# Optimization experiments

Hardware: AMD Instinct MI355X
Metric: run time of the kernel (lower is better)

Reference implementation:

```python
import jax, jax.numpy as jnp
import numpy as np

N = 32768          # total nodes
B = 64             # graphs
NPG = N // B       # nodes per graph (equal-sized graphs)
E = 524288         # edges (before self-loops)
D_IN, HID, HEADS, D_OUT = 128, 64, 4, 128
DH = HID * HEADS   # 256
NEG_SLOPE = 0.2
EPS = 1e-5

def _leaky(x):
    return jnp.where(x >= 0, x, NEG_SLOPE * x)

def gat_conv(x, src, dst, W, a_src, a_dst, b, concat):
    """PyG-style GATConv (self-loops already included in src/dst)."""
    H, C = a_src.shape
    h = (x @ W).reshape(N, H, C)                       # [N,H,C]
    es = jnp.einsum('nhc,hc->nh', h, a_src)            # score from source feats
    ed = jnp.einsum('nhc,hc->nh', h, a_dst)            # score from target feats
    e = _leaky(es[src] + ed[dst])                      # [E',H]
    m = jax.ops.segment_max(e, dst, num_segments=N)    # stable softmax per dst
    p = jnp.exp(e - m[dst])
    s = jax.ops.segment_sum(p, dst, num_segments=N)
    alpha = p / s[dst]                                 # [E',H]
    out = jax.ops.segment_sum(h[src] * alpha[..., None], dst, num_segments=N)
    out = out.reshape(N, H * C) if concat else out.mean(axis=1)
    return out + b

def mha(x, Wi, bi, Wo, bo, heads):
    """torch.nn.MultiheadAttention (batch_first, no mask, eval)."""
    Bb, T, D = x.shape
    qkv = x @ Wi.T + bi                                # [B,T,3D]
    q, k, v = jnp.split(qkv, 3, axis=-1)
    hd = D // heads
    def sp(t):
        return t.reshape(Bb, T, heads, hd).transpose(0, 2, 1, 3)  # [B,h,T,hd]
    q, k, v = sp(q), sp(k), sp(v)
    scores = jnp.einsum('bhqd,bhkd->bhqk', q, k) / jnp.sqrt(jnp.float32(hd))
    attn = jax.nn.softmax(scores, axis=-1)
    o = jnp.einsum('bhqk,bhkd->bhqd', attn, v)
    o = o.transpose(0, 2, 1, 3).reshape(Bb, T, D)
    return o @ Wo.T + bo

def layer_norm(x, g, b):
    mu = x.mean(-1, keepdims=True)
    var = x.var(-1, keepdims=True)
    return (x - mu) / jnp.sqrt(var + EPS) * g + b

def setup_inputs() -> dict:
    key = jax.random.key(0)
    ks = jax.random.split(key, 20)
    s = 0.1
    inp = {
        'x': jax.random.normal(ks[0], (N, D_IN), jnp.float32),
        'edge_index': jax.random.randint(ks[1], (2, E), 0, N, jnp.int64),
        'batch': (jnp.arange(N, dtype=jnp.int64) // NPG),
        # gat1: D_IN -> HEADS*HID (concat)
        'W1': jax.random.normal(ks[2], (D_IN, HEADS * HID), jnp.float32) * s,
        'aS1': jax.random.normal(ks[3], (HEADS, HID), jnp.float32) * s,
        'aD1': jax.random.normal(ks[4], (HEADS, HID), jnp.float32) * s,
        'b1': jnp.zeros((HEADS * HID,), jnp.float32),
        # gat2: DH -> HEADS*HID (concat)
        'W2': jax.random.normal(ks[5], (DH, HEADS * HID), jnp.float32) * s,
        'aS2': jax.random.normal(ks[6], (HEADS, HID), jnp.float32) * s,
        'aD2': jax.random.normal(ks[7], (HEADS, HID), jnp.float32) * s,
        'b2': jnp.zeros((HEADS * HID,), jnp.float32),
        # gat3: DH -> D_OUT, heads=1, concat=False (mean)
        'W3': jax.random.normal(ks[8], (DH, D_OUT), jnp.float32) * s,
        'aS3': jax.random.normal(ks[9], (1, D_OUT), jnp.float32) * s,
        'aD3': jax.random.normal(ks[10], (1, D_OUT), jnp.float32) * s,
        'b3': jnp.zeros((D_OUT,), jnp.float32),
        # MultiheadAttention
        'Wi': jax.random.normal(ks[11], (3 * DH, DH), jnp.float32) * s,
        'bi': jnp.zeros((3 * DH,), jnp.float32),
        'Wo': jax.random.normal(ks[12], (DH, DH), jnp.float32) * s,
        'bo': jnp.zeros((DH,), jnp.float32),
        # LayerNorm
        'gamma': jnp.ones((DH,), jnp.float32),
        'beta': jnp.zeros((DH,), jnp.float32),
    }
    return inp

def reference(x, edge_index, batch, W1, aS1, aD1, b1, W2, aS2, aD2, b2,
              W3, aS3, aD3, b3, Wi, bi, Wo, bo, gamma, beta):
    # add self-loops (PyG GATConv default)
    loops = jnp.arange(N, dtype=edge_index.dtype)
    src = jnp.concatenate([edge_index[0], loops])
    dst = jnp.concatenate([edge_index[1], loops])

    x1 = jax.nn.elu(gat_conv(x, src, dst, W1, aS1, aD1, b1, concat=True))
    x2 = jax.nn.elu(gat_conv(x1, src, dst, W2, aS2, aD2, b2, concat=True))

    # ragged-to-dense batching: batch = arange(N)//NPG (equal-sized, sorted),
    # so the torch python loop reduces to a reshape with no padding.
    x2b = x2.reshape(B, NPG, DH)
    attended = mha(x2b, Wi, bi, Wo, bo, HEADS).reshape(N, DH)

    x2a = layer_norm(attended + x2, gamma, beta)
    x3 = gat_conv(x2a, src, dst, W3, aS3, aD3, b3, concat=False)
    return x3
```

## Files before the change

### kernel.cpp

```cpp
#include <hip/hip_runtime.h>

typedef _Float16 half_t;
typedef _Float16 half8  __attribute__((ext_vector_type(8)));
typedef _Float16 half4v __attribute__((ext_vector_type(4)));
typedef float    f32x4  __attribute__((ext_vector_type(4)));

constexpr int N_NODES = 32768;
constexpr int NPG_    = 512;

#define MFMA16(a, b, c) __builtin_amdgcn_mfma_f32_16x16x32_f16((a), (b), (c), 0, 0, 0)

__device__ __forceinline__ void gload_lds16(const half_t* g, half_t* l) {
  __builtin_amdgcn_global_load_lds(
      (const __attribute__((address_space(1))) void*)g,
      (__attribute__((address_space(3))) void*)l, 16, 0, 0);
}

__global__ void k_hist(const int* __restrict__ dst, int* __restrict__ deg, int E) {
  int i = blockIdx.x * 256 + threadIdx.x;
  if (i < E) atomicAdd(&deg[dst[i]], 1);
}

__global__ __launch_bounds__(1024) void k_scan(const int* __restrict__ deg,
                                               int* __restrict__ rowptr) {
  __shared__ int part[1024];
  int t = threadIdx.x;
  int base = t * 32;
  int s = 0;
  #pragma unroll
  for (int i = 0; i < 32; i++) s += deg[base + i];
  part[t] = s;
  __syncthreads();
  for (int off = 1; off < 1024; off <<= 1) {
    int add = (t >= off) ? part[t - off] : 0;
    __syncthreads();
    part[t] += add;
    __syncthreads();
  }
  int run = (t == 0) ? 0 : part[t - 1];
  for (int i = 0; i < 32; i++) { rowptr[base + i] = run; run += deg[base + i]; }
  if (t == 1023) rowptr[N_NODES] = run;
}

__global__ void k_selfloop(const int* __restrict__ rowptr, int* __restrict__ fill,
                           int* __restrict__ col) {
  int i = blockIdx.x * 256 + threadIdx.x;
  fill[i] = 1;
  col[rowptr[i]] = i;
}

__global__ void k_scatter(const int* __restrict__ src, const int* __restrict__ dst,
                          const int* __restrict__ rowptr, int* __restrict__ fill,
                          int* __restrict__ col, int E) {
  int i = blockIdx.x * 256 + threadIdx.x;
  if (i < E) {
    int d = dst[i];
    int pos = rowptr[d] + atomicAdd(&fill[d], 1);
    col[pos] = src[i];
  }
}

__global__ void k_convert(
    const float* __restrict__ x,  half_t* __restrict__ x_h,
    const float* __restrict__ W1, half_t* __restrict__ W1t,
    const float* __restrict__ W2, half_t* __restrict__ W2t,
    const float* __restrict__ W3, half_t* __restrict__ W3t,
    const float* __restrict__ Wi, half_t* __restrict__ Wi_h,
    const float* __restrict__ Wo, half_t* __restrict__ Wo_h,
    int* __restrict__ deg)
{
  int bid = blockIdx.x, t = threadIdx.x;
  if (bid < 16384) {
    int i = bid * 256 + t;
    x_h[i] = (half_t)x[i];
  } else if (bid < 16512) {
    int i = (bid - 16384) * 256 + t;
    int o = i >> 7, k = i & 127;
    W1t[i] = (half_t)W1[k * 256 + o];
  } else if (bid < 16768) {
    int i = (bid - 16512) * 256 + t;
    int o = i >> 8, k = i & 255;
    W2t[i] = (half_t)W2[k * 256 + o];
  } else if (bid < 16896) {
    int i = (bid - 16768) * 256 + t;
    int o = i >> 8, k = i & 255;
    W3t[i] = (half_t)W3[k * 128 + o];
  } else if (bid < 17664) {
    int i = (bid - 16896) * 256 + t;
    Wi_h[i] = (half_t)Wi[i];
  } else if (bid < 17920) {
    int i = (bid - 17664) * 256 + t;
    Wo_h[i] = (half_t)Wo[i];
  } else {
    deg[(bid - 17920) * 256 + t] = 1;
  }
}

__global__ __launch_bounds__(256) void k_gemm(
    const half_t* __restrict__ A, const half_t* __restrict__ Bt,
    const float* __restrict__ bias, int bias_per_row,
    half_t* __restrict__ outh, float* __restrict__ outf,
    int M, int Nc, int K,
    const float* __restrict__ aS, const float* __restrict__ aD,
    float* __restrict__ es, float* __restrict__ ed, int H)
{
  __shared__ __align__(16) half_t As[128 * 64];
  __shared__ __align__(16) half_t Bs[128 * 64];
  __shared__ float sRed[2][4][64];
  int w = threadIdx.x >> 6, lane = threadIdx.x & 63;
  int r = lane & 15, q = lane >> 4;
  int m0 = blockIdx.y * 128, n0 = blockIdx.x * 128;
  int mh = (w & 1) * 64, nh = (w >> 1) * 64;
  f32x4 acc[4][4];
  #pragma unroll
  for (int i = 0; i < 4; i++)
    #pragma unroll
    for (int j = 0; j < 4; j++) acc[i][j] = f32x4{0.f, 0.f, 0.f, 0.f};

  int srow = lane >> 3;
  int sc   = lane & 7;

  for (int k0 = 0; k0 < K; k0 += 64) {
    __syncthreads();
    #pragma unroll
    for (int i = 0; i < 4; i++) {
      int R0 = w * 32 + i * 8;
      int row = R0 + srow;
      int cg = sc ^ (row & 7);
      gload_lds16(A  + (size_t)(m0 + row) * K + k0 + cg * 8, &As[R0 * 64]);
      gload_lds16(Bt + (size_t)(n0 + row) * K + k0 + cg * 8, &Bs[R0 * 64]);
    }
    __syncthreads();
    #pragma unroll
    for (int kk = 0; kk < 2; kk++) {
      half8 af[4], bf[4];
      #pragma unroll
      for (int t = 0; t < 4; t++) {
        int rr = mh + t * 16 + r;
        af[t] = *(const half8*)&As[rr * 64 + (((kk * 4 + q) ^ (rr & 7)) << 3)];
      }
      #pragma unroll
      for (int t = 0; t < 4; t++) {
        int rr = nh + t * 16 + r;
        bf[t] = *(const half8*)&Bs[rr * 64 + (((kk * 4 + q) ^ (rr & 7)) << 3)];
      }
      #pragma unroll
      for (int ti = 0; ti < 4; ti++)
        #pragma unroll
        for (int tj = 0; tj < 4; tj++)
          acc[ti][tj] = MFMA16(af[ti], bf[tj], acc[ti][tj]);
    }
  }

  #pragma unroll
  for (int tj = 0; tj < 4; tj++) {
    int colc = n0 + nh + tj * 16 + r;
    #pragma unroll
    for (int ti = 0; ti < 4; ti++) {
      #pragma unroll
      for (int i = 0; i < 4; i++) {
        int row = m0 + mh + ti * 16 + q * 4 + i;
        float bv = bias ? (bias_per_row ? bias[row] : bias[colc]) : 0.f;
        float v = acc[ti][tj][i] + bv;
        size_t idx = (size_t)row * Nc + colc;
        if (outf) outf[idx] = v;
        if (outh) outh[idx] = (half_t)v;
      }
    }
  }

  if (es) {
    if (H == 4) {
      int head = (n0 >> 6) + (nh >> 6);
      float aSv[4], aDv[4];
      #pragma unroll
      for (int tj = 0; tj < 4; tj++) {
        int cl = tj * 16 + r;
        aSv[tj] = aS[head * 64 + cl];
        aDv[tj] = aD[head * 64 + cl];
      }
      #pragma unroll
      for (int ti = 0; ti < 4; ti++) {
        #pragma unroll
        for (int i = 0; i < 4; i++) {
          float ps = 0.f, pd = 0.f;
          #pragma unroll
          for (int tj = 0; tj < 4; tj++) {
            float av = acc[ti][tj][i];
            ps += av * aSv[tj];
            pd += av * aDv[tj];
          }
          #pragma unroll
          for (int off = 1; off < 16; off <<= 1) {
            ps += __shfl_xor(ps, off);
            pd += __shfl_xor(pd, off);
          }
          if (r == 0) {
            int row = m0 + mh + ti * 16 + q * 4 + i;
            es[(size_t)row * 4 + head] = ps;
            ed[(size_t)row * 4 + head] = pd;
          }
        }
      }
    } else {
      float aSv[4], aDv[4];
      #pragma unroll
      for (int tj = 0; tj < 4; tj++) {
        int c = nh + tj * 16 + r;
        aSv[tj] = aS[c];
        aDv[tj] = aD[c];
      }
      #pragma unroll
      for (int ti = 0; ti < 4; ti++) {
        #pragma unroll
        for (int i = 0; i < 4; i++) {
          float ps = 0.f, pd = 0.f;
          #pragma unroll
          for (int tj = 0; tj < 4; tj++) {
            float av = acc[ti][tj][i];
            ps += av * aSv[tj];
            pd += av * aDv[tj];
          }
          #pragma unroll
          for (int off = 1; off < 16; off <<= 1) {
            ps += __shfl_xor(ps, off);
            pd += __shfl_xor(pd, off);
          }
          if (r == 0) {
            int ri = ti * 16 + q * 4 + i;
            sRed[0][w][ri] = ps;
            sRed[1][w][ri] = pd;
          }
        }
      }
      __syncthreads();
      if (threadIdx.x < 128) {
        int row = threadIdx.x;
        int wlo = row >> 6, ri = row & 63;
        es[m0 + row] = sRed[0][wlo][ri] + sRed[0][wlo + 2][ri];
        ed[m0 + row] = sRed[1][wlo][ri] + sRed[1][wlo + 2][ri];
      }
    }
  }
}

template<int HC, int H, bool FP16ACC>
__global__ __launch_bounds__(256) void k_agg(
    const half_t* __restrict__ h, const float* __restrict__ es,
    const float* __restrict__ ed, const float* __restrict__ bias,
    const int* __restrict__ rowptr, const int* __restrict__ col, int elu,
    float* __restrict__ outf, half_t* __restrict__ outh)
{
  constexpr int VPT = HC / 16;
  constexpr int NV8 = VPT / 8;
  constexpr int C = HC / H;
  int lane = threadIdx.x & 63;
  int g = lane >> 4, li = lane & 15;
  int n = blockIdx.x * 4 + (threadIdx.x >> 6);
  int cbase = li * VPT;
  int hl = cbase / C;
  float edn = ed[(size_t)n * H + hl];
  int j0 = rowptr[n], j1 = rowptr[n + 1];
  const half_t* hb = h + cbase;

  float sum0 = 0.f, sum1 = 0.f;

  if constexpr (FP16ACC) {
    half8 acc0[NV8], acc1[NV8];
    #pragma unroll
    for (int i = 0; i < NV8; i++) {
      acc0[i] = half8{0, 0, 0, 0, 0, 0, 0, 0};
      acc1[i] = half8{0, 0, 0, 0, 0, 0, 0, 0};
    }
    for (int j = j0 + g; j < j1; j += 8) {
      int jb = j + 4;
      int s0 = col[j];
      int s1 = col[(jb < j1) ? jb : j];
      float e0 = es[(size_t)s0 * H + hl] + edn;
      e0 = fmaxf(e0, 0.2f * e0);
      float e1 = es[(size_t)s1 * H + hl] + edn;
      e1 = fmaxf(e1, 0.2f * e1);
      e1 = (jb < j1) ? e1 : -1e30f;
      const half_t* hp0 = hb + (size_t)s0 * HC;
      const half_t* hp1 = hb + (size_t)s1 * HC;
      float p0 = __expf(e0 - 6.f), p1 = __expf(e1 - 6.f);
      sum0 += p0; sum1 += p1;
      half_t q0 = (half_t)p0, q1 = (half_t)p1;
      half8 pv0 = {q0, q0, q0, q0, q0, q0, q0, q0};
      half8 pv1 = {q1, q1, q1, q1, q1, q1, q1, q1};
      #pragma unroll
      for (int i = 0; i < NV8; i++) {
        half8 v0 = *(const half8*)(hp0 + i * 8);
        half8 v1 = *(const half8*)(hp1 + i * 8);
        acc0[i] += pv0 * v0;
        acc1[i] += pv1 * v1;
      }
    }
    float sum = sum0 + sum1;
    sum += __shfl_xor(sum, 16);
    sum += __shfl_xor(sum, 32);
    float av[VPT];
    #pragma unroll
    for (int i = 0; i < VPT; i++) {
      av[i] = (float)acc0[i >> 3][i & 7] + (float)acc1[i >> 3][i & 7];
      av[i] += __shfl_xor(av[i], 16);
      av[i] += __shfl_xor(av[i], 32);
    }
    float inv = 1.f / sum;
    float v[VPT];
    #pragma unroll
    for (int i = 0; i < VPT; i++) {
      float t = av[i] * inv + bias[cbase + i];
      if (elu) t = (t > 0.f) ? t : __expf(t) - 1.f;
      v[i] = t;
    }
    if (g == 0) {
      size_t obase = (size_t)n * HC + cbase;
      if (outh) {
        #pragma unroll
        for (int p8 = 0; p8 < NV8; p8++) {
          half8 hv;
          #pragma unroll
          for (int i = 0; i < 8; i++) hv[i] = (half_t)v[p8 * 8 + i];
          *(half8*)(outh + obase + p8 * 8) = hv;
        }
      }
      if (outf) {
        #pragma unroll
        for (int p4 = 0; p4 < VPT / 4; p4++) {
          float4 fv = {v[p4 * 4], v[p4 * 4 + 1], v[p4 * 4 + 2], v[p4 * 4 + 3]};
          *(float4*)(outf + obase + p4 * 4) = fv;
        }
      }
    }
  } else {
    float acc0[VPT], acc1[VPT];
    #pragma unroll
    for (int i = 0; i < VPT; i++) { acc0[i] = 0.f; acc1[i] = 0.f; }
    for (int j = j0 + g; j < j1; j += 8) {
      int jb = j + 4;
      int s0 = col[j];
      int s1 = col[(jb < j1) ? jb : j];
      float e0 = es[(size_t)s0 * H + hl] + edn;
      e0 = fmaxf(e0, 0.2f * e0);
      float e1 = es[(size_t)s1 * H + hl] + edn;
      e1 = fmaxf(e1, 0.2f * e1);
      e1 = (jb < j1) ? e1 : -1e30f;
      const half_t* hp0 = hb + (size_t)s0 * HC;
      const half_t* hp1 = hb + (size_t)s1 * HC;
      float p0 = __expf(e0), p1 = __expf(e1);
      sum0 += p0; sum1 += p1;
      #pragma unroll
      for (int c8 = 0; c8 < NV8; c8++) {
        half8 a0 = *(const half8*)(hp0 + c8 * 8);
        half8 a1 = *(const half8*)(hp1 + c8 * 8);
        #pragma unroll
        for (int i = 0; i < 8; i++) {
          acc0[c8 * 8 + i] += p0 * (float)a0[i];
          acc1[c8 * 8 + i] += p1 * (float)a1[i];
        }
      }
    }
    float sum = sum0 + sum1;
    sum += __shfl_xor(sum, 16);
    sum += __shfl_xor(sum, 32);
    float av[VPT];
    #pragma unroll
    for (int i = 0; i < VPT; i++) {
      av[i] = acc0[i] + acc1[i];
      av[i] += __shfl_xor(av[i], 16);
      av[i] += __shfl_xor(av[i], 32);
    }
    float inv = 1.f / sum;
    float v[VPT];
    #pragma unroll
    for (int i = 0; i < VPT; i++) {
      float t = av[i] * inv + bias[cbase + i];
      if (elu) t = (t > 0.f) ? t : __expf(t) - 1.f;
      v[i] = t;
    }
    if (g == 0) {
      size_t obase = (size_t)n * HC + cbase;
      if (outh) {
        #pragma unroll
        for (int p8 = 0; p8 < NV8; p8++) {
          half8 hv;
          #pragma unroll
          for (int i = 0; i < 8; i++) hv[i] = (half_t)v[p8 * 8 + i];
          *(half8*)(outh + obase + p8 * 8) = hv;
        }
      }
      if (outf) {
        #pragma unroll
        for (int p4 = 0; p4 < VPT / 4; p4++) {
          float4 fv = {v[p4 * 4], v[p4 * 4 + 1], v[p4 * 4 + 2], v[p4 * 4 + 3]};
          *(float4*)(outf + obase + p4 * 4) = fv;
        }
      }
    }
  }
}

__global__ __launch_bounds__(256) void k_attn(
    const half_t* __restrict__ qk, const half_t* __restrict__ vt,
    half_t* __restrict__ o)
{
  __shared__ __align__(16) half_t Kt[128 * 64];
  __shared__ __align__(16) half_t Vt[64 * 128];
  __shared__ __align__(16) half_t Pb[4][16][136];

  int pair = blockIdx.x;
  int b = pair >> 2, hh = pair & 3;
  int q0 = blockIdx.y * 64;
  int w = threadIdx.x >> 6, lane = threadIdx.x & 63;
  int cc = lane & 15, qq = lane >> 4;

  const half_t* Qp = qk + ((size_t)(b * NPG_ + q0 + w * 16 + cc) * 512 + hh * 64);
  half8 qa0 = *(const half8*)(Qp + qq * 8);
  half8 qa1 = *(const half8*)(Qp + 32 + qq * 8);

  f32x4 oacc[4];
  #pragma unroll
  for (int t = 0; t < 4; t++) oacc[t] = f32x4{0.f, 0.f, 0.f, 0.f};
  float rs = 0.f;

  const half_t* kb = qk + ((size_t)(b * NPG_) * 512 + 256 + hh * 64);
  const half_t* vb = vt + ((size_t)(hh * 64) * 32768 + b * NPG_);

  int krow_l = lane >> 3, ks_l = lane & 7;
  int vrow_l = lane >> 4, vs_l = lane & 15;

  for (int kt = 0; kt < 4; kt++) {
    __syncthreads();
    #pragma unroll
    for (int i = 0; i < 4; i++) {
      int R = (i * 4 + w) * 8;
      int kr = R + krow_l;
      gload_lds16(kb + (size_t)(kt * 128 + kr) * 512 + ((ks_l ^ (kr & 7)) * 8),
                  &Kt[R * 64]);
    }
    #pragma unroll
    for (int i = 0; i < 4; i++) {
      int D0 = (i * 4 + w) * 4;
      int d = D0 + vrow_l;
      gload_lds16(vb + (size_t)d * 32768 + kt * 128 + ((vs_l ^ (d & 15)) * 8),
                  &Vt[D0 * 128]);
    }
    __syncthreads();

    #pragma unroll
    for (int mt = 0; mt < 8; mt++) {
      int key = mt * 16 + cc;
      half8 k0 = *(const half8*)&Kt[key * 64 + ((qq ^ (key & 7)) << 3)];
      half8 k1 = *(const half8*)&Kt[key * 64 + (((qq + 4) ^ (key & 7)) << 3)];
      f32x4 s = f32x4{0.f, 0.f, 0.f, 0.f};
      s = MFMA16(k0, qa0, s);
      s = MFMA16(k1, qa1, s);
      half4v ph;
      #pragma unroll
      for (int i = 0; i < 4; i++) {
        float p = __expf(s[i] * 0.125f - 8.0f);
        rs += p;
        ph[i] = (half_t)p;
      }
      *(half4v*)&Pb[w][cc][mt * 16 + qq * 4] = ph;
    }

    #pragma unroll
    for (int kc = 0; kc < 4; kc++) {
      half8 a = *(const half8*)&Pb[w][cc][kc * 32 + qq * 8];
      #pragma unroll
      for (int nt = 0; nt < 4; nt++) {
        int d = nt * 16 + cc;
        half8 bb = *(const half8*)&Vt[d * 128 + (((kc * 4 + qq) ^ (d & 15)) << 3)];
        oacc[nt] = MFMA16(a, bb, oacc[nt]);
      }
    }
  }

  rs += __shfl_xor(rs, 16);
  rs += __shfl_xor(rs, 32);
  #pragma unroll
  for (int i = 0; i < 4; i++) {
    float rsv = __shfl(rs, qq * 4 + i);
    float inv = 1.f / rsv;
    int node = b * NPG_ + q0 + w * 16 + qq * 4 + i;
    #pragma unroll
    for (int nt = 0; nt < 4; nt++)
      o[(size_t)node * 256 + hh * 64 + nt * 16 + cc] = (half_t)(oacc[nt][i] * inv);
  }
}

__global__ __launch_bounds__(256) void k_ln(
    const half_t* __restrict__ att, const half_t* __restrict__ x2,
    const float* __restrict__ gamma, const float* __restrict__ beta,
    half_t* __restrict__ outh)
{
  int lane = threadIdx.x & 63;
  int n = blockIdx.x * 4 + (threadIdx.x >> 6);
  size_t base = (size_t)n * 256 + lane * 4;
  half4v a  = *(const half4v*)(att + base);
  half4v xx = *(const half4v*)(x2 + base);
  float v[4];
  #pragma unroll
  for (int i = 0; i < 4; i++) v[i] = (float)a[i] + (float)xx[i];
  float s  = v[0] + v[1] + v[2] + v[3];
  float ss = v[0]*v[0] + v[1]*v[1] + v[2]*v[2] + v[3]*v[3];
  #pragma unroll
  for (int off = 1; off < 64; off <<= 1) {
    s  += __shfl_xor(s, off);
    ss += __shfl_xor(ss, off);
  }
  float mean = s * (1.f / 256.f);
  float var  = ss * (1.f / 256.f) - mean * mean;
  float rstd = rsqrtf(var + 1e-5f);
  #pragma unroll
  for (int i = 0; i < 4; i++) {
    int c = lane * 4 + i;
    outh[(size_t)n * 256 + c] = (half_t)((v[i] - mean) * rstd * gamma[c] + beta[c]);
  }
}

extern "C" void kernel_launch(void* const* d_in, const int* in_sizes, int n_in,
                              void* d_out, int out_size, void* d_ws, size_t ws_size,
                              hipStream_t stream)
{
  const float* x    = (const float*)d_in[0];
  const int*   ei   = (const int*)d_in[1];
  const float* W1   = (const float*)d_in[3];
  const float* aS1  = (const float*)d_in[4];
  const float* aD1  = (const float*)d_in[5];
  const float* b1   = (const float*)d_in[6];
  const float* W2   = (const float*)d_in[7];
  const float* aS2  = (const float*)d_in[8];
  const float* aD2  = (const float*)d_in[9];
  const float* b2   = (const float*)d_in[10];
  const float* W3   = (const float*)d_in[11];
  const float* aS3  = (const float*)d_in[12];
  const float* aD3  = (const float*)d_in[13];
  const float* b3   = (const float*)d_in[14];
  const float* Wi   = (const float*)d_in[15];
  const float* bi   = (const float*)d_in[16];
  const float* Wo   = (const float*)d_in[17];
  const float* bo   = (const float*)d_in[18];
  const float* gam  = (const float*)d_in[19];
  const float* bet  = (const float*)d_in[20];
  float* out = (float*)d_out;
  const int N = N_NODES;
  int E = in_sizes[1] / 2;

  char* ws = (char*)d_ws;
  size_t off = 0;
  auto alloc = [&](size_t bytes) -> void* {
    void* p = ws + off;
    off = (off + bytes + 255) & ~(size_t)255;
    return p;
  };
  half_t* x_h    = (half_t*)alloc((size_t)N * 128 * 2);
  half_t* h_h    = (half_t*)alloc((size_t)N * 256 * 2);
  half_t* x1_h   = (half_t*)alloc((size_t)N * 256 * 2);
  half_t* x2_h   = (half_t*)alloc((size_t)N * 256 * 2);
  half_t* qk_h   = (half_t*)alloc((size_t)N * 512 * 2);
  half_t* vt_h   = (half_t*)alloc((size_t)256 * N * 2);
  half_t* o_h    = (half_t*)alloc((size_t)N * 256 * 2);
  half_t* att_h  = (half_t*)alloc((size_t)N * 256 * 2);
  half_t* x2a_h  = (half_t*)alloc((size_t)N * 256 * 2);
  half_t* W1t    = (half_t*)alloc(256 * 128 * 2);
  half_t* W2t    = (half_t*)alloc(256 * 256 * 2);
  half_t* W3t    = (half_t*)alloc(128 * 256 * 2);
  half_t* Wi_h   = (half_t*)alloc(768 * 256 * 2);
  half_t* Wo_h   = (half_t*)alloc(256 * 256 * 2);
  float*  es     = (float*) alloc((size_t)N * 4 * 4);
  float*  ed     = (float*) alloc((size_t)N * 4 * 4);
  int*    deg    = (int*)   alloc((size_t)N * 4);
  int*    fill   = (int*)   alloc((size_t)N * 4);
  int*    rowptr = (int*)   alloc(((size_t)N + 1) * 4);
  int*    col    = (int*)   alloc((size_t)(N + E) * 4);

  const int* srcE = ei;
  const int* dstE = ei + E;

  k_convert<<<18048, 256, 0, stream>>>(x, x_h, W1, W1t, W2, W2t, W3, W3t,
                                       Wi, Wi_h, Wo, Wo_h, deg);
  k_hist<<<(E + 255) / 256, 256, 0, stream>>>(dstE, deg, E);
  k_scan<<<1, 1024, 0, stream>>>(deg, rowptr);
  k_selfloop<<<N / 256, 256, 0, stream>>>(rowptr, fill, col);
  k_scatter<<<(E + 255) / 256, 256, 0, stream>>>(srcE, dstE, rowptr, fill, col, E);

  k_gemm<<<dim3(2, N / 128), 256, 0, stream>>>(x_h, W1t, nullptr, 0, h_h, nullptr,
                                               N, 256, 128, aS1, aD1, es, ed, 4);
  k_agg<256, 4, true><<<N / 4, 256, 0, stream>>>(h_h, es, ed, b1, rowptr, col, 1, nullptr, x1_h);

  k_gemm<<<dim3(2, N / 128), 256, 0, stream>>>(x1_h, W2t, nullptr, 0, h_h, nullptr,
                                               N, 256, 256, aS2, aD2, es, ed, 4);
  k_agg<256, 4, true><<<N / 4, 256, 0, stream>>>(h_h, es, ed, b2, rowptr, col, 1, nullptr, x2_h);

  k_gemm<<<dim3(4, N / 128), 256, 0, stream>>>(x2_h, Wi_h, bi, 0, qk_h, nullptr,
                                               N, 512, 256, nullptr, nullptr, nullptr, nullptr, 0);
  k_gemm<<<dim3(N / 128, 2), 256, 0, stream>>>(Wi_h + 512 * 256, x2_h, bi + 512, 1,
                                               vt_h, nullptr, 256, N, 256,
                                               nullptr, nullptr, nullptr, nullptr, 0);
  k_attn<<<dim3(256, 8), 256, 0, stream>>>(qk_h, vt_h, o_h);
  k_gemm<<<dim3(2, N / 128), 256, 0, stream>>>(o_h, Wo_h, bo, 0, att_h, nullptr,
                                               N, 256, 256, nullptr, nullptr, nullptr, nullptr, 0);

  k_ln<<<N / 4, 256, 0, stream>>>(att_h, x2_h, gam, bet, x2a_h);

  k_gemm<<<dim3(1, N / 128), 256, 0, stream>>>(x2a_h, W3t, nullptr, 0, h_h, nullptr,
                                               N, 128, 256, aS3, aD3, es, ed, 1);
  k_agg<128, 1, false><<<N / 4, 256, 0, stream>>>(h_h, es, ed, b3, rowptr, col, 0, out, nullptr);
}
```

Measured before the change: 460.0 us.

## Fuse output projection with residual LayerNorm and widen attention query tiles

Adds a k_gemm_ln kernel that runs the Wo projection, adds bias and the residual, and applies LayerNorm in the epilogue with a cross-wave reduction in shared memory. This removes the separate LN kernel and the att_h round trip. The attention kernel now gives each wave four 16-query subtiles, so each K/V tile loaded into LDS is reused across 256 queries per block instead of 64, at the cost of more accumulator registers and fewer blocks. The exponentials are rewritten as exp2f with pre-scaled constants in both attention and aggregation.

```diff
diff --git a/kernel.cpp b/kernel.cpp
--- a/kernel.cpp
+++ b/kernel.cpp
@@ -244,6 +244,123 @@
   }
 }
 
+__global__ __launch_bounds__(256) void k_gemm_ln(
+    const half_t* __restrict__ A, const half_t* __restrict__ Bt,
+    const float* __restrict__ bias, const half_t* __restrict__ res,
+    const float* __restrict__ gamma, const float* __restrict__ beta,
+    half_t* __restrict__ outh)
+{
+  __shared__ __align__(16) half_t As[64 * 64];
+  __shared__ __align__(16) half_t Bs[256 * 64];
+  __shared__ float sSum[4][64], sSq[4][64];
+  __shared__ float sMR[64][2];
+  int w = threadIdx.x >> 6, lane = threadIdx.x & 63;
+  int r = lane & 15, q = lane >> 4;
+  int m0 = blockIdx.x * 64;
+  int nh = w * 64;
+  f32x4 acc[4][4];
+  #pragma unroll
+  for (int i = 0; i < 4; i++)
+    #pragma unroll
+    for (int j = 0; j < 4; j++) acc[i][j] = f32x4{0.f, 0.f, 0.f, 0.f};
+
+  int srow = lane >> 3, sc = lane & 7;
+
+  for (int k0 = 0; k0 < 256; k0 += 64) {
+    __syncthreads();
+    #pragma unroll
+    for (int i = 0; i < 2; i++) {
+      int R0 = w * 16 + i * 8;
+      int row = R0 + srow;
+      int cg = sc ^ (row & 7);
+      gload_lds16(A + (size_t)(m0 + row) * 256 + k0 + cg * 8, &As[R0 * 64]);
+    }
+    #pragma unroll
+    for (int i = 0; i < 8; i++) {
+      int R0 = w * 64 + i * 8;
+      int row = R0 + srow;
+      int cg = sc ^ (row & 7);
+      gload_lds16(Bt + (size_t)row * 256 + k0 + cg * 8, &Bs[R0 * 64]);
+    }
+    __syncthreads();
+    #pragma unroll
+    for (int kk = 0; kk < 2; kk++) {
+      half8 af[4], bf[4];
+      #pragma unroll
+      for (int t = 0; t < 4; t++) {
+        int rr = t * 16 + r;
+        af[t] = *(const half8*)&As[rr * 64 + (((kk * 4 + q) ^ (rr & 7)) << 3)];
+      }
+      #pragma unroll
+      for (int t = 0; t < 4; t++) {
+        int rr = nh + t * 16 + r;
+        bf[t] = *(const half8*)&Bs[rr * 64 + (((kk * 4 + q) ^ (rr & 7)) << 3)];
+      }
+      #pragma unroll
+      for (int ti = 0; ti < 4; ti++)
+        #pragma unroll
+        for (int tj = 0; tj < 4; tj++)
+          acc[ti][tj] = MFMA16(af[ti], bf[tj], acc[ti][tj]);
+    }
+  }
+
+  float gv[4], bv[4];
+  #pragma unroll
+  for (int tj = 0; tj < 4; tj++) {
+    int col = nh + tj * 16 + r;
+    gv[tj] = gamma[col];
+    bv[tj] = beta[col];
+  }
+  #pragma unroll
+  for (int ti = 0; ti < 4; ti++) {
+    #pragma unroll
+    for (int i = 0; i < 4; i++) {
+      int row = ti * 16 + q * 4 + i;
+      float s = 0.f, ss = 0.f;
+      #pragma unroll
+      for (int tj = 0; tj < 4; tj++) {
+        int col = nh + tj * 16 + r;
+        float v = acc[ti][tj][i] + bias[col]
+                + (float)res[(size_t)(m0 + row) * 256 + col];
+        acc[ti][tj][i] = v;
+        s += v;
+        ss += v * v;
+      }
+      #pragma unroll
+      for (int off = 1; off < 16; off <<= 1) {
+        s  += __shfl_xor(s, off);
+        ss += __shfl_xor(ss, off);
+      }
+      if (r == 0) { sSum[w][row] = s; sSq[w][row] = ss; }
+    }
+  }
+  __syncthreads();
+  if (threadIdx.x < 64) {
+    int row = threadIdx.x;
+    float s  = sSum[0][row] + sSum[1][row] + sSum[2][row] + sSum[3][row];
+    float ss = sSq[0][row] + sSq[1][row] + sSq[2][row] + sSq[3][row];
+    float mean = s * (1.f / 256.f);
+    float var  = ss * (1.f / 256.f) - mean * mean;
+    sMR[row][0] = mean;
+    sMR[row][1] = rsqrtf(var + 1e-5f);
+  }
+  __syncthreads();
+  #pragma unroll
+  for (int ti = 0; ti < 4; ti++) {
+    #pragma unroll
+    for (int i = 0; i < 4; i++) {
+      int row = ti * 16 + q * 4 + i;
+      float mean = sMR[row][0], rstd = sMR[row][1];
+      #pragma unroll
+      for (int tj = 0; tj < 4; tj++) {
+        int col = nh + tj * 16 + r;
+        outh[(size_t)(m0 + row) * 256 + col] =
+            (half_t)((acc[ti][tj][i] - mean) * rstd * gv[tj] + bv[tj]);
+      }
+    }
+  }
+}
+
 template<int HC, int H, bool FP16ACC>
 __global__ __launch_bounds__(256) void k_agg(
     const half_t* __restrict__ h, const float* __restrict__ es,
@@ -283,7 +400,8 @@
       e1 = (jb < j1) ? e1 : -1e30f;
       const half_t* hp0 = hb + (size_t)s0 * HC;
       const half_t* hp1 = hb + (size_t)s1 * HC;
-      float p0 = __expf(e0 - 6.f), p1 = __expf(e1 - 6.f);
+      float p0 = exp2f(e0 * 1.44269504f - 8.65617025f);
+      float p1 = exp2f(e1 * 1.44269504f - 8.65617025f);
       sum0 += p0; sum1 += p1;
       half_t q0 = (half_t)p0, q1 = (half_t)p1;
       half8 pv0 = {q0, q0, q0, q0, q0, q0, q0, q0};
@@ -411,18 +529,25 @@
 
   int pair = blockIdx.x;
   int b = pair >> 2, hh = pair & 3;
-  int q0 = blockIdx.y * 64;
+  int q0 = blockIdx.y * 256;
   int w = threadIdx.x >> 6, lane = threadIdx.x & 63;
   int cc = lane & 15, qq = lane >> 4;
-
-  const half_t* Qp = qk + ((size_t)(b * NPG_ + q0 + w * 16 + cc) * 512 + hh * 64);
-  half8 qa0 = *(const half8*)(Qp + qq * 8);
-  half8 qa1 = *(const half8*)(Qp + 32 + qq * 8);
-
-  f32x4 oacc[4];
-  #pragma unroll
-  for (int t = 0; t < 4; t++) oacc[t] = f32x4{0.f, 0.f, 0.f, 0.f};
-  float rs = 0.f;
+  int qb = q0 + w * 64;
+
+  half8 qa0[4], qa1[4];
+  #pragma unroll
+  for (int qs = 0; qs < 4; qs++) {
+    const half_t* Qp = qk + ((size_t)(b * NPG_ + qb + qs * 16 + cc) * 512 + hh * 64);
+    qa0[qs] = *(const half8*)(Qp + qq * 8);
+    qa1[qs] = *(const half8*)(Qp + 32 + qq * 8);
+  }
+
+  f32x4 oacc[4][4];
+  #pragma unroll
+  for (int a = 0; a < 4; a++)
+    #pragma unroll
+    for (int t = 0; t < 4; t++) oacc[a][t] = f32x4{0.f, 0.f, 0.f, 0.f};
+  float rs[4] = {0.f, 0.f, 0.f, 0.f};
 
   const half_t* kb = qk + ((size_t)(b * NPG_) * 512 + 256 + hh * 64);
   const half_t* vb = vt + ((size_t)(hh * 64) * 32768 + b * NPG_);
@@ -449,75 +574,51 @@
     __syncthreads();
 
     #pragma unroll
-    for (int mt = 0; mt < 8; mt++) {
-      int key = mt * 16 + cc;
-      half8 k0 = *(const half8*)&Kt[key * 64 + ((qq ^ (key & 7)) << 3)];
-      half8 k1 = *(const half8*)&Kt[key * 64 + (((qq + 4) ^ (key & 7)) << 3)];
-      f32x4 s = f32x4{0.f, 0.f, 0.f, 0.f};
-      s = MFMA16(k0, qa0, s);
-      s = MFMA16(k1, qa1, s);
-      half4v ph;
-      #pragma unroll
-      for (int i = 0; i < 4; i++) {
-        float p = __expf(s[i] * 0.125f - 8.0f);
-        rs += p;
-        ph[i] = (half_t)p;
-      }
-      *(half4v*)&Pb[w][cc][mt * 16 + qq * 4] = ph;
-    }
-
-    #pragma unroll
-    for (int kc = 0; kc < 4; kc++) {
-      half8 a = *(const half8*)&Pb[w][cc][kc * 32 + qq * 8];
-      #pragma unroll
-      for (int nt = 0; nt < 4; nt++) {
-        int d = nt * 16 + cc;
-        half8 bb = *(const half8*)&Vt[d * 128 + (((kc * 4 + qq) ^ (d & 15)) << 3)];
-        oacc[nt] = MFMA16(a, bb, oacc[nt]);
-      }
-    }
-  }
-
-  rs += __shfl_xor(rs, 16);
-  rs += __shfl_xor(rs, 32);
-  #pragma unroll
-  for (int i = 0; i < 4; i++) {
-    float rsv = __shfl(rs, qq * 4 + i);
-    float inv = 1.f / rsv;
-    int node = b * NPG_ + q0 + w * 16 + qq * 4 + i;
-    #pragma unroll
-    for (int nt = 0; nt < 4; nt++)
-      o[(size_t)node * 256 + hh * 64 + nt * 16 + cc] = (half_t)(oacc[nt][i] * inv);
-  }
-}
-
-__global__ __launch_bounds__(256) void k_ln(
-    const half_t* __restrict__ att, const half_t* __restrict__ x2,
-    const float* __restrict__ gamma, const float* __restrict__ beta,
-    half_t* __restrict__ outh)
-{
-  int lane = threadIdx.x & 63;
-  int n = blockIdx.x * 4 + (threadIdx.x >> 6);
-  size_t base = (size_t)n * 256 + lane * 4;
-  half4v a  = *(const half4v*)(att + base);
-  half4v xx = *(const half4v*)(x2 + base);
-  float v[4];
-  #pragma unroll
-  for (int i = 0; i < 4; i++) v[i] = (float)a[i] + (float)xx[i];
-  float s  = v[0] + v[1] + v[2] + v[3];
-  float ss = v[0]*v[0] + v[1]*v[1] + v[2]*v[2] + v[3]*v[3];
-  #pragma unroll
-  for (int off = 1; off < 64; off <<= 1) {
-    s  += __shfl_xor(s, off);
-    ss += __shfl_xor(ss, off);
-  }
-  float mean = s * (1.f / 256.f);
-  float var  = ss * (1.f / 256.f) - mean * mean;
-  float rstd = rsqrtf(var + 1e-5f);
-  #pragma unroll
-  for (int i = 0; i < 4; i++) {
-    int c = lane * 4 + i;
-    outh[(size_t)n * 256 + c] = (half_t)((v[i] - mean) * rstd * gamma[c] + beta[c]);
+    for (int qs = 0; qs < 4; qs++) {
+      #pragma unroll
+      for (int mt = 0; mt < 8; mt++) {
+        int key = mt * 16 + cc;
+        half8 k0 = *(const half8*)&Kt[key * 64 + ((qq ^ (key & 7)) << 3)];
+        half8 k1 = *(const half8*)&Kt[key * 64 + (((qq + 4) ^ (key & 7)) << 3)];
+        f32x4 s = f32x4{0.f, 0.f, 0.f, 0.f};
+        s = MFMA16(k0, qa0[qs], s);
+        s = MFMA16(k1, qa1[qs], s);
+        half4v ph;
+        #pragma unroll
+        for (int i = 0; i < 4; i++) {
+          float p = exp2f(s[i] * 0.180336886f - 11.54156033f);
+          rs[qs] += p;
+          ph[i] = (half_t)p;
+        }
+        *(half4v*)&Pb[w][cc][mt * 16 + qq * 4] = ph;
+      }
+      #pragma unroll
+      for (int kc = 0; kc < 4; kc++) {
+        half8 a = *(const half8*)&Pb[w][cc][kc * 32 + qq * 8];
+        #pragma unroll
+        for (int nt = 0; nt < 4; nt++) {
+          int d = nt * 16 + cc;
+          half8 bb = *(const half8*)&Vt[d * 128 + (((kc * 4 + qq) ^ (d & 15)) << 3)];
+          oacc[qs][nt] = MFMA16(a, bb, oacc[qs][nt]);
+        }
+      }
+    }
+  }
+
+  #pragma unroll
+  for (int qs = 0; qs < 4; qs++) {
+    float r = rs[qs];
+    r += __shfl_xor(r, 16);
+    r += __shfl_xor(r, 32);
+    #pragma unroll
+    for (int i = 0; i < 4; i++) {
+      float rsv = __shfl(r, qq * 4 + i);
+      float inv = 1.f / rsv;
+      int node = b * NPG_ + qb + qs * 16 + qq * 4 + i;
+      #pragma unroll
+      for (int nt = 0; nt < 4; nt++)
+        o[(size_t)node * 256 + hh * 64 + nt * 16 + cc] = (half_t)(oacc[qs][nt][i] * inv);
+    }
   }
 }
 
@@ -563,7 +664,6 @@
   half_t* qk_h   = (half_t*)alloc((size_t)N * 512 * 2);
   half_t* vt_h   = (half_t*)alloc((size_t)256 * N * 2);
   half_t* o_h    = (half_t*)alloc((size_t)N * 256 * 2);
-  half_t* att_h  = (half_t*)alloc((size_t)N * 256 * 2);
   half_t* x2a_h  = (half_t*)alloc((size_t)N * 256 * 2);
   half_t* W1t    = (half_t*)alloc(256 * 128 * 2);
   half_t* W2t    = (half_t*)alloc(256 * 256 * 2);
@@ -600,11 +700,9 @@
   k_gemm<<<dim3(N / 128, 2), 256, 0, stream>>>(Wi_h + 512 * 256, x2_h, bi + 512, 1,
                                                vt_h, nullptr, 256, N, 256,
                                                nullptr, nullptr, nullptr, nullptr, 0);
-  k_attn<<<dim3(256, 8), 256, 0, stream>>>(qk_h, vt_h, o_h);
-  k_gemm<<<dim3(2, N / 128), 256, 0, stream>>>(o_h, Wo_h, bo, 0, att_h, nullptr,
-                                               N, 256, 256, nullptr, nullptr, nullptr, nullptr, 0);
-
-  k_ln<<<N / 4, 256, 0, stream>>>(att_h, x2_h, gam, bet, x2a_h);
+  k_attn<<<dim3(256, 2), 256, 0, stream>>>(qk_h, vt_h, o_h);
+
+  k_gemm_ln<<<N / 64, 256, 0, stream>>>(o_h, Wo_h, bo, x2_h, gam, bet, x2a_h);
 
   k_gemm<<<dim3(1, N / 128), 256, 0, stream>>>(x2a_h, W3t, nullptr, 0, h_h, nullptr,
                                                N, 128, 256, aS3, aD3, es, ed, 1);
```

New measurement: 448.3 us. 2.5% less time.
